# Optimization experiments

Hardware: AMD Instinct MI355X
Metric: run time of the kernel (lower is better)

## Reference

```python
import jax, jax.numpy as jnp
import numpy as np

N, E, F_IN, H, O = 50000, 800000, 128, 8, 8  # nodes, edges, in_feat, heads, out-per-head
NEG_SLOPE = 0.2

def setup_inputs() -> dict:
    key = jax.random.key(0)
    k1, k2, k3, k4, k5, k6 = jax.random.split(key, 6)
    h = jax.random.normal(k1, (N, F_IN), dtype=jnp.float32)
    # xavier_uniform-like scale (gain=1.414) expressed via normal init scale
    w_scale = 1.414 * np.sqrt(2.0 / (F_IN + O)).astype(np.float32)
    W = jax.random.normal(k2, (H, F_IN, O), dtype=jnp.float32) * w_scale
    a_scale = 1.414 * np.sqrt(2.0 / (2 * O + 1)).astype(np.float32)
    a1 = jax.random.normal(k3, (H, O), dtype=jnp.float32) * a_scale
    a2 = jax.random.normal(k4, (H, O), dtype=jnp.float32) * a_scale
    src = jax.random.randint(k5, (E,), 0, N, dtype=jnp.int64 if jax.config.jax_enable_x64 else jnp.int32)
    dst = jax.random.randint(k6, (E,), 0, N, dtype=jnp.int64 if jax.config.jax_enable_x64 else jnp.int32)
    return {"h": h, "W": W, "a1": a1, "a2": a2, "src": src, "dst": dst}

def reference(h, W, a1, a2, src, dst):
    # Per-head linear projection: [N, H, O]
    Wh = jnp.einsum('nf,hfo->nho', h, W)
    # Per-node attention half-scores (a split into src/dst halves): [N, H]
    s_src = jnp.einsum('nho,ho->nh', Wh, a1)
    s_dst = jnp.einsum('nho,ho->nh', Wh, a2)
    # Edge attention logits: [E, H]
    e = jax.nn.leaky_relu(s_src[src] + s_dst[dst], negative_slope=NEG_SLOPE)
    # Numerically-stable segment softmax over incoming edges of each dst node
    m = jax.ops.segment_max(e, dst, num_segments=N)          # [N, H]
    m = jnp.where(jnp.isfinite(m), m, jnp.float32(0.0))      # isolated nodes -> 0
    p = jnp.exp(e - m[dst])                                   # [E, H]
    denom = jax.ops.segment_sum(p, dst, num_segments=N)       # [N, H]
    attn = p / jnp.maximum(denom[dst], jnp.float32(1e-16))    # [E, H]
    # Weighted scatter-sum of messages: [N, H, O]
    out = jax.ops.segment_sum(attn[:, :, None] * Wh[src], dst, num_segments=N)
    # Concatenate heads: [N, H*O]
    return out.reshape(N, H * O)
```

## Files before the change

kernel.cpp:

```cpp
#include <hip/hip_runtime.h>
#include <hip/hip_bf16.h>
#include <hip/hip_fp16.h>


#define FIN 128
#define NH 8
#define NO 8
#define NC 64
#define NB_COLS 80
#define GR 64
#define EPB 4096
#define BCAP 8192

typedef __attribute__((ext_vector_type(8))) short bf16x8;
typedef __attribute__((ext_vector_type(4))) float f32x4;

static __device__ __forceinline__ unsigned short f2bf(float f) {
    unsigned u = __float_as_uint(f);
    u += 0x7fff + ((u >> 16) & 1);
    return (unsigned short)(u >> 16);
}

__global__ __launch_bounds__(256) void prep_kernel(
    const float* __restrict__ W, const float* __restrict__ a1, const float* __restrict__ a2,
    unsigned short* __restrict__ wBg, int* __restrict__ bcnt)
{
    const int t = threadIdx.x;
    bcnt[t] = 0;
    for (int i = t; i < NH * FIN * NO; i += 256) {
        int hh = i >> 10, f = (i >> 3) & 127, o = i & 7;
        int c = hh * 8 + o;
        wBg[c * FIN + (f ^ ((c & 7) << 3))] = f2bf(W[i]);
    }
    for (int i = t; i < 16 * FIN; i += 256) {
        int j = i >> 7;
        int f = i & 127;
        int hh = j & 7;
        const float* av = (j < 8) ? (a1 + hh * NO) : (a2 + hh * NO);
        const float* wv = W + hh * (FIN * NO) + f * NO;
        float s = 0.f;
#pragma unroll
        for (int o = 0; o < 8; ++o) s += wv[o] * av[o];
        int c = 64 + j;
        wBg[c * FIN + (f ^ ((c & 7) << 3))] = f2bf(s);
    }
}

__global__ __launch_bounds__(256) void gemm_s_scat_kernel(
    const float* __restrict__ h, const unsigned short* __restrict__ wBg,
    const int* __restrict__ src, const int* __restrict__ dst,
    int* __restrict__ bcnt, unsigned* __restrict__ packed,
    __half* __restrict__ Wh, float* __restrict__ s_src, float* __restrict__ s_dst,
    int N, int E, int gemm_blocks)
{
    __shared__ alignas(16) unsigned short wB[NB_COLS * FIN];
    __shared__ int cnt_l[256];
    __shared__ int base_l[256];
    const int tid = threadIdx.x;

    if (blockIdx.x >= gemm_blocks) {
        const long e0 = (long)(blockIdx.x - gemm_blocks) * EPB;
        cnt_l[tid] = 0;
        __syncthreads();
        int br[16];
        unsigned pk[16];
#pragma unroll
        for (int j = 0; j < 16; ++j) {
            long e = e0 + j * 256 + tid;
            bool ok = (e < E);
            int d = ok ? dst[e] : 0;
            int s = ok ? src[e] : 0;
            int b = d >> 8;
            int r = ok ? atomicAdd(&cnt_l[b], 1) : 0;
            br[j] = ok ? ((b << 16) | r) : -1;
            pk[j] = ((unsigned)(d & 255) << 16) | (unsigned)s;
        }
        __syncthreads();
        if (cnt_l[tid] > 0) base_l[tid] = atomicAdd(&bcnt[tid], cnt_l[tid]);
        __syncthreads();
#pragma unroll
        for (int j = 0; j < 16; ++j) {
            if (br[j] >= 0) {
                int b = br[j] >> 16, r = br[j] & 0xFFFF;
                packed[(long)b * BCAP + base_l[b] + r] = pk[j];
            }
        }
        return;
    }

    const int w    = tid >> 6;
    const int lane = tid & 63;
    const int l15  = lane & 15;
    const int lg   = lane >> 4;

    const int row  = blockIdx.x * GR + w * 16 + l15;
    const int rowc = (row < N) ? row : (N - 1);
    const float* hrow = h + (long)rowc * FIN + lg * 8;
    float4 va[8];
#pragma unroll
    for (int kk = 0; kk < 4; ++kk) {
        va[2 * kk]     = *(const float4*)(hrow + kk * 32);
        va[2 * kk + 1] = *(const float4*)(hrow + kk * 32 + 4);
    }

    {
        const uint4* s4 = (const uint4*)wBg;
        uint4* d4 = (uint4*)wB;
#pragma unroll
        for (int j = 0; j < 5; ++j)
            d4[j * 256 + tid] = s4[j * 256 + tid];
    }
    __syncthreads();

    bf16x8 af[4];
#pragma unroll
    for (int kk = 0; kk < 4; ++kk) {
        bf16x8 r;
        r[0] = (short)f2bf(va[2 * kk].x);     r[1] = (short)f2bf(va[2 * kk].y);
        r[2] = (short)f2bf(va[2 * kk].z);     r[3] = (short)f2bf(va[2 * kk].w);
        r[4] = (short)f2bf(va[2 * kk + 1].x); r[5] = (short)f2bf(va[2 * kk + 1].y);
        r[6] = (short)f2bf(va[2 * kk + 1].z); r[7] = (short)f2bf(va[2 * kk + 1].w);
        af[kk] = r;
    }

    f32x4 acc[5] = {{0,0,0,0},{0,0,0,0},{0,0,0,0},{0,0,0,0},{0,0,0,0}};
#pragma unroll
    for (int kk = 0; kk < 4; ++kk) {
        int kb = kk * 64 + lg * 16;
#pragma unroll
        for (int nt = 0; nt < 5; ++nt) {
            int c = nt * 16 + l15;
            bf16x8 bf = *(const bf16x8*)((const char*)wB + c * (FIN * 2) + (kb ^ ((c & 7) << 4)));
            acc[nt] = __builtin_amdgcn_mfma_f32_16x16x32_bf16(af[kk], bf, acc[nt], 0, 0, 0);
        }
    }

    const int row0 = blockIdx.x * GR;
#pragma unroll
    for (int nt = 0; nt < 4; ++nt) {
        int col = nt * 16 + l15;
#pragma unroll
        for (int r = 0; r < 4; ++r) {
            int n = row0 + w * 16 + lg * 4 + r;
            if (n < N) Wh[(long)n * NC + col] = __float2half_rn(acc[nt][r]);
        }
    }
#pragma unroll
    for (int r = 0; r < 4; ++r) {
        int n = row0 + w * 16 + lg * 4 + r;
        if (n < N) {
            float v = acc[4][r];
            if (l15 < 8) s_src[n * NH + l15] = v;
            else         s_dst[n * NH + (l15 - 8)] = v;
        }
    }
}

__global__ __launch_bounds__(256) void bucketB_kernel(
    const unsigned* __restrict__ packed, const int* __restrict__ bcnt,
    int* __restrict__ row_off, unsigned short* __restrict__ srcs,
    int N, int E, int nb)
{
    __shared__ int bins[256];
    __shared__ int scan_s[256];
    __shared__ int g0s;
    __shared__ unsigned short outb[BCAP];
    const int t = threadIdx.x;
    const int b = blockIdx.x;
    const int d0 = b << 8;
    const unsigned* pin = packed + (long)b * BCAP;

    int v2 = (t < nb) ? bcnt[t] : 0;
    scan_s[t] = v2;
    __syncthreads();
    for (int off = 1; off < 256; off <<= 1) {
        int u = (t >= off) ? scan_s[t - off] : 0;
        __syncthreads();
        scan_s[t] += u;
        __syncthreads();
    }
    if (t == b) g0s = scan_s[t] - v2;
    bins[t] = 0;
    __syncthreads();
    const int g0 = g0s;
    const int cnt = bcnt[b];

    for (int i = t; i < cnt; i += 256)
        atomicAdd(&bins[pin[i] >> 16], 1);
    __syncthreads();
    int v = bins[t];
    scan_s[t] = v;
    __syncthreads();
    for (int off = 1; off < 256; off <<= 1) {
        int u = (t >= off) ? scan_s[t - off] : 0;
        __syncthreads();
        scan_s[t] += u;
        __syncthreads();
    }
    if (d0 + t < N) row_off[d0 + t] = g0 + scan_s[t] - v;
    if (b == nb - 1 && t == 0) row_off[N] = E;
    bins[t] = scan_s[t] - v;
    __syncthreads();
    for (int i = t; i < cnt; i += 256) {
        unsigned p = pin[i];
        int pos = atomicAdd(&bins[p >> 16], 1);
        outb[pos] = (unsigned short)(p & 0xFFFF);
    }
    __syncthreads();
    for (int i = t; i < cnt; i += 256)
        srcs[g0 + i] = outb[i];
}

__global__ __launch_bounds__(256) void gather_kernel(
    const unsigned short* __restrict__ srcs, const int* __restrict__ row_off,
    const float* __restrict__ s_src, const float* __restrict__ s_dst,
    const __half* __restrict__ Wh, float* __restrict__ out, int N)
{
    int wid = blockIdx.x * 4 + (threadIdx.x >> 6);
    if (wid >= N) return;
    const int lane = threadIdx.x & 63;
    const int el = lane >> 3;
    const int hh = lane & 7;
    int beg = row_off[wid];
    int end = row_off[wid + 1];
    float sd = s_dst[wid * NH + hh];
    float acc = 0.f, den = 0.f;

    for (int i = beg; i < end; i += 8) {
        int idx = i + el;
        bool val = (idx < end);
        int s = (int)srcs[val ? idx : beg];
        float ss = s_src[s * NH + hh];
        float x = ss + sd;
        x = (x > 0.f) ? x : 0.2f * x;
        float p = __expf(x);
        p = val ? p : 0.f;
        den += p;
#pragma unroll
        for (int k = 0; k < 8; ++k) {
            int sk   = __shfl(s, k * 8);
            float pk = __shfl(p, k * 8 + (lane >> 3));
            float wv = __half2float(Wh[((unsigned)sk << 6) | (unsigned)lane]);
            acc = fmaf(pk, wv, acc);
        }
    }
    den += __shfl_xor(den, 8);
    den += __shfl_xor(den, 16);
    den += __shfl_xor(den, 32);
    float den_b = __shfl(den, lane >> 3);
    out[(unsigned)wid * NC + (unsigned)lane] = acc / fmaxf(den_b, 1e-16f);
}

extern "C" void kernel_launch(void* const* d_in, const int* in_sizes, int n_in,
                              void* d_out, int out_size, void* d_ws, size_t ws_size,
                              hipStream_t stream)
{
    const float* h  = (const float*)d_in[0];
    const float* W  = (const float*)d_in[1];
    const float* a1 = (const float*)d_in[2];
    const float* a2 = (const float*)d_in[3];
    const int*  src = (const int*)d_in[4];
    const int*  dst = (const int*)d_in[5];
    float* out = (float*)d_out;

    const int N = in_sizes[0] / FIN;
    const int E = in_sizes[4];
    const int nb = (N + 255) >> 8;

    char* wsb = (char*)d_ws;
    __half* Wh         = (__half*)wsb;           wsb += (size_t)N * NC * 2;
    float* s_src       = (float*)wsb;            wsb += (size_t)N * NH * 4;
    float* s_dst       = (float*)wsb;            wsb += (size_t)N * NH * 4;
    int* row_off       = (int*)wsb;              wsb += (size_t)(N + 1) * 4;
    int* bcnt          = (int*)wsb;              wsb += (size_t)256 * 4;
    unsigned short* wBg = (unsigned short*)wsb;  wsb += (size_t)NB_COLS * FIN * 2;
    unsigned* packed   = (unsigned*)wsb;         wsb += (size_t)nb * BCAP * 4;
    unsigned short* srcs = (unsigned short*)wsb; wsb += (size_t)E * 2;

    prep_kernel<<<1, 256, 0, stream>>>(W, a1, a2, wBg, bcnt);

    const int gemm_blocks = (N + GR - 1) / GR;
    const int scat_blocks = (E + EPB - 1) / EPB;
    gemm_s_scat_kernel<<<gemm_blocks + scat_blocks, 256, 0, stream>>>(
        h, wBg, src, dst, bcnt, packed, Wh, s_src, s_dst, N, E, gemm_blocks);

    bucketB_kernel<<<nb, 256, 0, stream>>>(packed, bcnt, row_off, srcs, N, E, nb);

    int g_blocks = (N + 3) / 4;
    gather_kernel<<<g_blocks, 256, 0, stream>>>(srcs, row_off, s_src, s_dst, Wh, out, N);
}
```

Measured before the change: 70.71 us.

## Fuse bucket sort into gather kernel and read GEMM weights directly from global

```diff
diff --git a/kernel.cpp b/kernel.cpp
--- a/kernel.cpp
+++ b/kernel.cpp
@@ -11,6 +11,7 @@
 #define GR 64
 #define EPB 4096
 #define BCAP 8192
+#define QCAP 2048
 
 typedef __attribute__((ext_vector_type(8))) short bf16x8;
 typedef __attribute__((ext_vector_type(4))) float f32x4;
@@ -30,7 +31,7 @@
     for (int i = t; i < NH * FIN * NO; i += 256) {
         int hh = i >> 10, f = (i >> 3) & 127, o = i & 7;
         int c = hh * 8 + o;
-        wBg[c * FIN + (f ^ ((c & 7) << 3))] = f2bf(W[i]);
+        wBg[c * FIN + f] = f2bf(W[i]);
     }
     for (int i = t; i < 16 * FIN; i += 256) {
         int j = i >> 7;
@@ -41,8 +42,7 @@
         float s = 0.f;
 #pragma unroll
         for (int o = 0; o < 8; ++o) s += wv[o] * av[o];
-        int c = 64 + j;
-        wBg[c * FIN + (f ^ ((c & 7) << 3))] = f2bf(s);
+        wBg[(64 + j) * FIN + f] = f2bf(s);
     }
 }
 
@@ -53,7 +53,6 @@
     __half* __restrict__ Wh, float* __restrict__ s_src, float* __restrict__ s_dst,
     int N, int E, int gemm_blocks)
 {
-    __shared__ alignas(16) unsigned short wB[NB_COLS * FIN];
     __shared__ int cnt_l[256];
     __shared__ int base_l[256];
     const int tid = threadIdx.x;
@@ -103,15 +102,6 @@
         va[2 * kk + 1] = *(const float4*)(hrow + kk * 32 + 4);
     }
 
-    {
-        const uint4* s4 = (const uint4*)wBg;
-        uint4* d4 = (uint4*)wB;
-#pragma unroll
-        for (int j = 0; j < 5; ++j)
-            d4[j * 256 + tid] = s4[j * 256 + tid];
-    }
-    __syncthreads();
-
     bf16x8 af[4];
 #pragma unroll
     for (int kk = 0; kk < 4; ++kk) {
@@ -126,11 +116,11 @@
     f32x4 acc[5] = {{0,0,0,0},{0,0,0,0},{0,0,0,0},{0,0,0,0},{0,0,0,0}};
 #pragma unroll
     for (int kk = 0; kk < 4; ++kk) {
-        int kb = kk * 64 + lg * 16;
+        const int k0 = kk * 32 + lg * 8;
 #pragma unroll
         for (int nt = 0; nt < 5; ++nt) {
             int c = nt * 16 + l15;
-            bf16x8 bf = *(const bf16x8*)((const char*)wB + c * (FIN * 2) + (kb ^ ((c & 7) << 4)));
+            bf16x8 bf = *(const bf16x8*)(wBg + c * FIN + k0);
             acc[nt] = __builtin_amdgcn_mfma_f32_16x16x32_bf16(af[kk], bf, acc[nt], 0, 0, 0);
         }
     }
@@ -156,99 +146,92 @@
     }
 }
 
-__global__ __launch_bounds__(256) void bucketB_kernel(
+__global__ __launch_bounds__(256) void sort_gather_kernel(
     const unsigned* __restrict__ packed, const int* __restrict__ bcnt,
-    int* __restrict__ row_off, unsigned short* __restrict__ srcs,
-    int N, int E, int nb)
-{
-    __shared__ int bins[256];
-    __shared__ int scan_s[256];
-    __shared__ int g0s;
-    __shared__ unsigned short outb[BCAP];
+    const float* __restrict__ s_src, const float* __restrict__ s_dst,
+    const __half* __restrict__ Wh, float* __restrict__ out, int N)
+{
+    __shared__ int cum[65];
+    __shared__ int cur[64];
+    __shared__ unsigned short srcs_l[QCAP];
     const int t = threadIdx.x;
-    const int b = blockIdx.x;
-    const int d0 = b << 8;
-    const unsigned* pin = packed + (long)b * BCAP;
-
-    int v2 = (t < nb) ? bcnt[t] : 0;
-    scan_s[t] = v2;
-    __syncthreads();
-    for (int off = 1; off < 256; off <<= 1) {
-        int u = (t >= off) ? scan_s[t - off] : 0;
-        __syncthreads();
-        scan_s[t] += u;
-        __syncthreads();
-    }
-    if (t == b) g0s = scan_s[t] - v2;
-    bins[t] = 0;
-    __syncthreads();
-    const int g0 = g0s;
-    const int cnt = bcnt[b];
-
-    for (int i = t; i < cnt; i += 256)
-        atomicAdd(&bins[pin[i] >> 16], 1);
-    __syncthreads();
-    int v = bins[t];
-    scan_s[t] = v;
-    __syncthreads();
-    for (int off = 1; off < 256; off <<= 1) {
-        int u = (t >= off) ? scan_s[t - off] : 0;
-        __syncthreads();
-        scan_s[t] += u;
-        __syncthreads();
-    }
-    if (d0 + t < N) row_off[d0 + t] = g0 + scan_s[t] - v;
-    if (b == nb - 1 && t == 0) row_off[N] = E;
-    bins[t] = scan_s[t] - v;
-    __syncthreads();
+    const int B = blockIdx.x >> 2;
+    const int q = blockIdx.x & 3;
+    const int d0 = (B << 8) + (q << 6);
+    const int cnt = bcnt[B];
+    const unsigned* pin = packed + (long)B * BCAP;
+
+    if (t < 64) cur[t] = 0;
+    __syncthreads();
+
     for (int i = t; i < cnt; i += 256) {
         unsigned p = pin[i];
-        int pos = atomicAdd(&bins[p >> 16], 1);
-        outb[pos] = (unsigned short)(p & 0xFFFF);
-    }
-    __syncthreads();
-    for (int i = t; i < cnt; i += 256)
-        srcs[g0 + i] = outb[i];
-}
-
-__global__ __launch_bounds__(256) void gather_kernel(
-    const unsigned short* __restrict__ srcs, const int* __restrict__ row_off,
-    const float* __restrict__ s_src, const float* __restrict__ s_dst,
-    const __half* __restrict__ Wh, float* __restrict__ out, int N)
-{
-    int wid = blockIdx.x * 4 + (threadIdx.x >> 6);
-    if (wid >= N) return;
-    const int lane = threadIdx.x & 63;
-    const int el = lane >> 3;
-    const int hh = lane & 7;
-    int beg = row_off[wid];
-    int end = row_off[wid + 1];
-    float sd = s_dst[wid * NH + hh];
-    float acc = 0.f, den = 0.f;
-
-    for (int i = beg; i < end; i += 8) {
-        int idx = i + el;
-        bool val = (idx < end);
-        int s = (int)srcs[val ? idx : beg];
-        float ss = s_src[s * NH + hh];
-        float x = ss + sd;
-        x = (x > 0.f) ? x : 0.2f * x;
-        float p = __expf(x);
-        p = val ? p : 0.f;
-        den += p;
-#pragma unroll
-        for (int k = 0; k < 8; ++k) {
-            int sk   = __shfl(s, k * 8);
-            float pk = __shfl(p, k * 8 + (lane >> 3));
-            float wv = __half2float(Wh[((unsigned)sk << 6) | (unsigned)lane]);
-            acc = fmaf(pk, wv, acc);
-        }
-    }
-    den += __shfl_xor(den, 8);
-    den += __shfl_xor(den, 16);
-    den += __shfl_xor(den, 32);
-    float den_b = __shfl(den, lane >> 3);
-    out[(unsigned)wid * NC + (unsigned)lane] = acc / fmaxf(den_b, 1e-16f);
+        int dl = p >> 16;
+        if ((dl >> 6) == q) atomicAdd(&cur[dl & 63], 1);
+    }
+    __syncthreads();
+
+    if (t < 64) {
+        int bv = cur[t];
+        int v = bv;
+#pragma unroll
+        for (int off = 1; off < 64; off <<= 1) {
+            int u = __shfl_up(v, off);
+            if (t >= off) v += u;
+        }
+        int excl = v - bv;
+        cum[t] = excl;
+        cur[t] = excl;
+        if (t == 63) cum[64] = v;
+    }
+    __syncthreads();
+
+    for (int i = t; i < cnt; i += 256) {
+        unsigned p = pin[i];
+        int dl = p >> 16;
+        if ((dl >> 6) == q) {
+            int pos = atomicAdd(&cur[dl & 63], 1);
+            if (pos < QCAP) srcs_l[pos] = (unsigned short)(p & 0xFFFF);
+        }
+    }
+    __syncthreads();
+
+    const int w    = t >> 6;
+    const int lane = t & 63;
+    const int el   = lane >> 3;
+    const int hh   = lane & 7;
+    for (int j = 0; j < 16; ++j) {
+        int ln = w + j * 4;
+        int d = d0 + ln;
+        if (d >= N) break;
+        int beg = cum[ln];
+        int end = cum[ln + 1];
+        float sd = s_dst[d * NH + hh];
+        float acc = 0.f, den = 0.f;
+        for (int i = beg; i < end; i += 8) {
+            int idx = i + el;
+            bool val = (idx < end);
+            int s = (int)srcs_l[val ? idx : beg];
+            float ss = s_src[s * NH + hh];
+            float x = ss + sd;
+            x = (x > 0.f) ? x : 0.2f * x;
+            float p = __expf(x);
+            p = val ? p : 0.f;
+            den += p;
+#pragma unroll
+            for (int k = 0; k < 8; ++k) {
+                int sk   = __shfl(s, k * 8);
+                float pk = __shfl(p, k * 8 + (lane >> 3));
+                float wv = __half2float(Wh[((unsigned)sk << 6) | (unsigned)lane]);
+                acc = fmaf(pk, wv, acc);
+            }
+        }
+        den += __shfl_xor(den, 8);
+        den += __shfl_xor(den, 16);
+        den += __shfl_xor(den, 32);
+        float den_b = __shfl(den, lane >> 3);
+        out[(unsigned)d * NC + (unsigned)lane] = acc / fmaxf(den_b, 1e-16f);
+    }
 }
 
 extern "C" void kernel_launch(void* const* d_in, const int* in_sizes, int n_in,
@@ -271,11 +254,9 @@
     __half* Wh         = (__half*)wsb;           wsb += (size_t)N * NC * 2;
     float* s_src       = (float*)wsb;            wsb += (size_t)N * NH * 4;
     float* s_dst       = (float*)wsb;            wsb += (size_t)N * NH * 4;
-    int* row_off       = (int*)wsb;              wsb += (size_t)(N + 1) * 4;
     int* bcnt          = (int*)wsb;              wsb += (size_t)256 * 4;
     unsigned short* wBg = (unsigned short*)wsb;  wsb += (size_t)NB_COLS * FIN * 2;
     unsigned* packed   = (unsigned*)wsb;         wsb += (size_t)nb * BCAP * 4;
-    unsigned short* srcs = (unsigned short*)wsb; wsb += (size_t)E * 2;
 
     prep_kernel<<<1, 256, 0, stream>>>(W, a1, a2, wBg, bcnt);
 
@@ -284,8 +265,6 @@
     gemm_s_scat_kernel<<<gemm_blocks + scat_blocks, 256, 0, stream>>>(
         h, wBg, src, dst, bcnt, packed, Wh, s_src, s_dst, N, E, gemm_blocks);
 
-    bucketB_kernel<<<nb, 256, 0, stream>>>(packed, bcnt, row_off, srcs, N, E, nb);
-
-    int g_blocks = (N + 3) / 4;
-    gather_kernel<<<g_blocks, 256, 0, stream>>>(srcs, row_off, s_src, s_dst, Wh, out, N);
-}
+    sort_gather_kernel<<<nb * 4, 256, 0, stream>>>(
+        packed, bcnt, s_src, s_dst, Wh, out, N);
+}
```

Result: slower. 83.90 us (+18.7%).
